# Performance work log

Hardware: AMD Instinct MI355X
Metric: run time of the kernel (lower is better)

## Reference

```python
import jax, jax.numpy as jnp
import numpy as np
import math

D_MODEL = 512
NUM_HEADS = 8
D_K = D_MODEL // NUM_HEADS
B, S = 8, 2048


def setup_inputs() -> dict:
    key = jax.random.key(0)
    ks = jax.random.split(key, 13)
    inv = 1.0 / math.sqrt(D_MODEL)
    def lin(kw, kb):
        W = jax.random.uniform(kw, (D_MODEL, D_MODEL), jnp.float32, -inv, inv)
        b = jax.random.uniform(kb, (D_MODEL,), jnp.float32, -inv, inv)
        return W, b
    Wq, bq = lin(ks[0], ks[1])
    Wk, bk = lin(ks[2], ks[3])
    Wv, bv = lin(ks[4], ks[5])
    Wo, bo = lin(ks[6], ks[7])
    Q = jax.random.normal(ks[8], (B, S, D_MODEL), jnp.float32)
    K = jax.random.normal(ks[9], (B, S, D_MODEL), jnp.float32)
    V = jax.random.normal(ks[10], (B, S, D_MODEL), jnp.float32)
    mask = jax.random.randint(ks[11], (1, 1, S, S), 0, 2, jnp.int32)
    return {"Q": Q, "K": K, "V": V, "mask": mask,
            "Wq": Wq, "bq": bq, "Wk": Wk, "bk": bk,
            "Wv": Wv, "bv": bv, "Wo": Wo, "bo": bo}


def _split_heads(x):
    b, s, _ = x.shape
    return x.reshape(b, s, NUM_HEADS, D_K).transpose(0, 2, 1, 3)  # [B,H,S,dk]


def reference(Q, K, V, mask, Wq, bq, Wk, bk, Wv, bv, Wo, bo):
    # Linear projections (torch Linear: x @ W^T + b) then head split
    q = _split_heads(Q @ Wq.T + bq)
    k = _split_heads(K @ Wk.T + bk)
    v = _split_heads(V @ Wv.T + bv)
    scores = jnp.einsum("bhqd,bhkd->bhqk", q, k) / math.sqrt(D_K)
    # masked_fill(mask == 0, -1e30) for float32
    scores = jnp.where(mask == 0, jnp.float32(-1e30), scores)
    probs = jax.nn.softmax(scores, axis=-1)
    # dropout in eval mode == identity
    out = jnp.einsum("bhqk,bhkd->bhqd", probs, v)
    out = out.transpose(0, 2, 1, 3).reshape(Q.shape[0], -1, D_MODEL)
    return out @ Wo.T + bo
```

## Files before the change

kernel.cpp:

```cpp
#include <hip/hip_runtime.h>
#include <hip/hip_bf16.h>
#include <math.h>

#define BB 8
#define SS 2048
#define HH 8
#define DKK 64
#define DM 512

typedef short bf16x8 __attribute__((ext_vector_type(8)));
typedef short bf16x4 __attribute__((ext_vector_type(4)));
typedef float f32x4 __attribute__((ext_vector_type(4)));
#define MFMA16(a, b, c) __builtin_amdgcn_mfma_f32_16x16x32_bf16(a, b, c, 0, 0, 0)

#if __has_builtin(__builtin_amdgcn_exp2f)
#define EXP2(x) __builtin_amdgcn_exp2f(x)
#else
#define EXP2(x) exp2f(x)
#endif

__device__ __forceinline__ unsigned short f2bf(float f) {
    __hip_bfloat16 h = __float2bfloat16(f);
    return *reinterpret_cast<unsigned short*>(&h);
}

__device__ __forceinline__ uint4 cvt8(const float* __restrict__ src) {
    float4 a = *(const float4*)src;
    float4 b = *(const float4*)(src + 4);
    unsigned short tmp[8];
    tmp[0] = f2bf(a.x); tmp[1] = f2bf(a.y); tmp[2] = f2bf(a.z); tmp[3] = f2bf(a.w);
    tmp[4] = f2bf(b.x); tmp[5] = f2bf(b.y); tmp[6] = f2bf(b.z); tmp[7] = f2bf(b.w);
    return *(uint4*)tmp;
}

__global__ __launch_bounds__(256) void mask_pack(
    const int* __restrict__ mask, unsigned long long* __restrict__ mb)
{
    const int t = threadIdx.x;
    const int wid = (blockIdx.x << 2) | (t >> 6);
    const int lane = t & 63;
    const int q = wid >> 5;
    const int c = wid & 31;
    int e = mask[(size_t)q * SS + (c << 6) + lane];
    unsigned long long bal = __ballot(e != 0);
    if (lane == 0) mb[wid] = bal;
}

__global__ __launch_bounds__(256, 2) void proj_qkv_fused(
    const float* __restrict__ Xq, const float* __restrict__ Xk, const float* __restrict__ Xv,
    const float* __restrict__ Wq, const float* __restrict__ Wk, const float* __restrict__ Wv,
    const float* __restrict__ bq, const float* __restrict__ bk, const float* __restrict__ bv,
    unsigned short* __restrict__ outbase, float qscale)
{
    const int z = blockIdx.z;
    const float* X = (z == 0) ? Xq : (z == 1) ? Xk : Xv;
    const float* W = (z == 0) ? Wq : (z == 1) ? Wk : Wv;
    const float* bias = (z == 0) ? bq : (z == 1) ? bk : bv;
    unsigned short* out = outbase + (size_t)z * ((size_t)BB * HH * SS * DKK);
    const float scale = (z == 0) ? qscale : 1.0f;

    __shared__ __align__(16) unsigned short Xs[128][72];
    __shared__ __align__(16) unsigned short Ws[128][72];
    const int t = threadIdx.x;
    const int w = t >> 6, l = t & 63;
    const int l15 = l & 15, lg = l >> 4;
    const int n0 = blockIdx.x * 128, m0 = blockIdx.y * 128;
    const int mo = (w & 1) * 64, no = (w >> 1) * 64;

    f32x4 acc[4][4];
#pragma unroll
    for (int i = 0; i < 4; i++)
#pragma unroll
        for (int j = 0; j < 4; j++) acc[i][j] = (f32x4){0.f, 0.f, 0.f, 0.f};

    for (int k0 = 0; k0 < DM; k0 += 64) {
        __syncthreads();
#pragma unroll
        for (int rr = 0; rr < 4; rr++) {
            int idx = rr * 2048 + t * 8;
            int row = idx >> 6, col = idx & 63;
            *(uint4*)&Xs[row][col] = cvt8(X + (size_t)(m0 + row) * DM + k0 + col);
            *(uint4*)&Ws[row][col] = cvt8(W + (size_t)(n0 + row) * DM + k0 + col);
        }
        __syncthreads();

        bf16x8 af[4][2], bfr[4][2];
#pragma unroll
        for (int mt = 0; mt < 4; mt++) {
            af[mt][0] = *(const bf16x8*)&Xs[mo + mt * 16 + l15][lg * 8];
            af[mt][1] = *(const bf16x8*)&Xs[mo + mt * 16 + l15][32 + lg * 8];
        }
#pragma unroll
        for (int nt = 0; nt < 4; nt++) {
            bfr[nt][0] = *(const bf16x8*)&Ws[no + nt * 16 + l15][lg * 8];
            bfr[nt][1] = *(const bf16x8*)&Ws[no + nt * 16 + l15][32 + lg * 8];
        }
#pragma unroll
        for (int mt = 0; mt < 4; mt++)
#pragma unroll
            for (int nt = 0; nt < 4; nt++) {
                acc[mt][nt] = MFMA16(af[mt][0], bfr[nt][0], acc[mt][nt]);
                acc[mt][nt] = MFMA16(af[mt][1], bfr[nt][1], acc[mt][nt]);
            }
    }

    float bv4[4];
#pragma unroll
    for (int nt = 0; nt < 4; nt++) bv4[nt] = bias[n0 + no + nt * 16 + l15];

    const int h = (n0 + no) >> 6;
    if (z == 2) {
#pragma unroll
        for (int mt = 0; mt < 4; mt++) {
            int m = m0 + mo + mt * 16 + lg * 4;
            int bb = m >> 11, s = m & (SS - 1);
#pragma unroll
            for (int nt = 0; nt < 4; nt++) {
                int d = nt * 16 + l15;
                bf16x4 pk;
#pragma unroll
                for (int r = 0; r < 4; r++) pk[r] = (short)f2bf(acc[mt][nt][r] + bv4[nt]);
                *(bf16x4*)(out + (((size_t)bb * HH + h) * DKK + d) * SS + s) = pk;
            }
        }
    } else {
#pragma unroll
        for (int mt = 0; mt < 4; mt++)
#pragma unroll
            for (int nt = 0; nt < 4; nt++)
#pragma unroll
                for (int r = 0; r < 4; r++) {
                    int m = m0 + mo + mt * 16 + lg * 4 + r;
                    int d = nt * 16 + l15;
                    float v = (acc[mt][nt][r] + bv4[nt]) * scale;
                    int bb = m >> 11, s = m & (SS - 1);
                    out[(((size_t)bb * HH + h) * SS + s) * 64 + d] = f2bf(v);
                }
    }
}

__global__ __launch_bounds__(256, 2) void proj_out_mfma(
    const unsigned short* __restrict__ Xb,
    const float* __restrict__ W,
    const float* __restrict__ bias,
    float* __restrict__ out)
{
    __shared__ __align__(16) unsigned short Xs[128][72];
    __shared__ __align__(16) unsigned short Ws[128][72];
    const int t = threadIdx.x;
    const int w = t >> 6, l = t & 63;
    const int l15 = l & 15, lg = l >> 4;
    const int n0 = blockIdx.x * 128, m0 = blockIdx.y * 128;
    const int mo = (w & 1) * 64, no = (w >> 1) * 64;

    f32x4 acc[4][4];
#pragma unroll
    for (int i = 0; i < 4; i++)
#pragma unroll
        for (int j = 0; j < 4; j++) acc[i][j] = (f32x4){0.f, 0.f, 0.f, 0.f};

    for (int k0 = 0; k0 < DM; k0 += 64) {
        __syncthreads();
#pragma unroll
        for (int rr = 0; rr < 4; rr++) {
            int idx = rr * 2048 + t * 8;
            int row = idx >> 6, col = idx & 63;
            *(uint4*)&Xs[row][col] = *(const uint4*)(Xb + (size_t)(m0 + row) * DM + k0 + col);
            *(uint4*)&Ws[row][col] = cvt8(W + (size_t)(n0 + row) * DM + k0 + col);
        }
        __syncthreads();

        bf16x8 af[4][2], bfr[4][2];
#pragma unroll
        for (int mt = 0; mt < 4; mt++) {
            af[mt][0] = *(const bf16x8*)&Xs[mo + mt * 16 + l15][lg * 8];
            af[mt][1] = *(const bf16x8*)&Xs[mo + mt * 16 + l15][32 + lg * 8];
        }
#pragma unroll
        for (int nt = 0; nt < 4; nt++) {
            bfr[nt][0] = *(const bf16x8*)&Ws[no + nt * 16 + l15][lg * 8];
            bfr[nt][1] = *(const bf16x8*)&Ws[no + nt * 16 + l15][32 + lg * 8];
        }
#pragma unroll
        for (int mt = 0; mt < 4; mt++)
#pragma unroll
            for (int nt = 0; nt < 4; nt++) {
                acc[mt][nt] = MFMA16(af[mt][0], bfr[nt][0], acc[mt][nt]);
                acc[mt][nt] = MFMA16(af[mt][1], bfr[nt][1], acc[mt][nt]);
            }
    }

    float bv4[4];
#pragma unroll
    for (int nt = 0; nt < 4; nt++) bv4[nt] = bias[n0 + no + nt * 16 + l15];

#pragma unroll
    for (int mt = 0; mt < 4; mt++)
#pragma unroll
        for (int nt = 0; nt < 4; nt++)
#pragma unroll
            for (int r = 0; r < 4; r++) {
                int m = m0 + mo + mt * 16 + lg * 4 + r;
                int n = n0 + no + nt * 16 + l15;
                out[(size_t)m * DM + n] = acc[mt][nt][r] + bv4[nt];
            }
}

__global__ __launch_bounds__(256, 2) void attn_kernel(
    const unsigned short* __restrict__ qw, const unsigned short* __restrict__ kw,
    const unsigned short* __restrict__ vtw,
    const unsigned long long* __restrict__ mb,
    unsigned short* __restrict__ ao)
{
    __shared__ __align__(16) unsigned short Ks[64][72];
    __shared__ __align__(16) unsigned short Vt[64][72];
    __shared__ __align__(16) unsigned short Pw[4 * 64 * 64];
    const int t = threadIdx.x;
    const int w = t >> 6, l = t & 63;
    const int l15 = l & 15, lg = l >> 4;
    const int q0 = blockIdx.x * 256;
    const int bh = blockIdx.y;
    const int b = bh >> 3, h = bh & 7;
    const int q0w = q0 + w * 64;
    const unsigned short* qb = qw + (size_t)bh * SS * DKK;
    const unsigned short* kb = kw + (size_t)bh * SS * DKK;
    const unsigned short* vtb = vtw + (size_t)bh * DKK * SS;

    const unsigned long long* mbq[4];
#pragma unroll
    for (int qt = 0; qt < 4; qt++)
        mbq[qt] = mb + ((size_t)(q0w + qt * 16 + l15) << 5);

    bf16x8 Qf[4][2];
#pragma unroll
    for (int qt = 0; qt < 4; qt++)
#pragma unroll
        for (int dh = 0; dh < 2; dh++)
            Qf[qt][dh] = *(const bf16x8*)(qb + (size_t)(q0w + qt * 16 + l15) * DKK + dh * 32 + lg * 8);

    f32x4 O[4][4];
#pragma unroll
    for (int i = 0; i < 4; i++)
#pragma unroll
        for (int j = 0; j < 4; j++) O[i][j] = (f32x4){0.f, 0.f, 0.f, 0.f};
    float m_i[4], l_i[4];
#pragma unroll
    for (int i = 0; i < 4; i++) { m_i[i] = -INFINITY; l_i[i] = 0.f; }

    const int pbase = w * 4096;

    for (int kv0 = 0; kv0 < SS; kv0 += 64) {
        __syncthreads();
#pragma unroll
        for (int r = 0; r < 2; r++) {
            int idx = r * 2048 + t * 8;
            int row = idx >> 6, col = idx & 63;
            *(uint4*)&Ks[row][col] = *(const uint4*)(kb + (size_t)(kv0 + row) * DKK + col);
            *(uint4*)&Vt[row][col] = *(const uint4*)(vtb + (size_t)row * SS + kv0 + col);
        }
        __syncthreads();

        f32x4 S[4][4];
#pragma unroll
        for (int kvt = 0; kvt < 4; kvt++) {
            bf16x8 ak0 = *(const bf16x8*)&Ks[kvt * 16 + l15][lg * 8];
            bf16x8 ak1 = *(const bf16x8*)&Ks[kvt * 16 + l15][32 + lg * 8];
#pragma unroll
            for (int qt = 0; qt < 4; qt++) {
                f32x4 z = (f32x4){0.f, 0.f, 0.f, 0.f};
                z = MFMA16(ak0, Qf[qt][0], z);
                z = MFMA16(ak1, Qf[qt][1], z);
                S[kvt][qt] = z;
            }
        }

#pragma unroll
        for (int qt = 0; qt < 4; qt++) {
            unsigned long long mm = mbq[qt][kv0 >> 6];
            unsigned int wlo = (unsigned int)mm;
            unsigned int whi = (unsigned int)(mm >> 32);
            unsigned int u[4];
            u[0] = wlo >> (lg * 4);
            u[1] = wlo >> (16 + lg * 4);
            u[2] = whi >> (lg * 4);
            u[3] = whi >> (16 + lg * 4);
#pragma unroll
            for (int kvt = 0; kvt < 4; kvt++) {
                if (!(u[kvt] & 1u)) S[kvt][qt][0] = -1e38f;
                if (!(u[kvt] & 2u)) S[kvt][qt][1] = -1e38f;
                if (!(u[kvt] & 4u)) S[kvt][qt][2] = -1e38f;
                if (!(u[kvt] & 8u)) S[kvt][qt][3] = -1e38f;
            }
        }

        float mtl[4];
#pragma unroll
        for (int qt = 0; qt < 4; qt++) {
            float mt = S[0][qt][0];
#pragma unroll
            for (int kvt = 0; kvt < 4; kvt++)
#pragma unroll
                for (int r = 0; r < 4; r++) mt = fmaxf(mt, S[kvt][qt][r]);
            mt = fmaxf(mt, __shfl_xor(mt, 16));
            mt = fmaxf(mt, __shfl_xor(mt, 32));
            mtl[qt] = mt;
        }
        int grow = (mtl[0] > m_i[0]) | (mtl[1] > m_i[1]) |
                   (mtl[2] > m_i[2]) | (mtl[3] > m_i[3]);
        if (__any(grow)) {
            float alpha[4];
#pragma unroll
            for (int qt = 0; qt < 4; qt++) {
                float mn = fmaxf(m_i[qt], mtl[qt]);
                alpha[qt] = EXP2(m_i[qt] - mn);
                m_i[qt] = mn;
                l_i[qt] *= alpha[qt];
            }
#pragma unroll
            for (int qt = 0; qt < 4; qt++)
#pragma unroll
                for (int r = 0; r < 4; r++) {
                    float a = __shfl(alpha[qt], lg * 4 + r);
#pragma unroll
                    for (int dt = 0; dt < 4; dt++) O[qt][dt][r] *= a;
                }
        }

#pragma unroll
        for (int qt = 0; qt < 4; qt++) {
            float ls = 0.f;
            const int prow = qt * 16 + l15;
            const int swz = (prow & 7) << 3;
#pragma unroll
            for (int kvt = 0; kvt < 4; kvt++) {
                float p0 = EXP2(S[kvt][qt][0] - m_i[qt]);
                float p1 = EXP2(S[kvt][qt][1] - m_i[qt]);
                float p2 = EXP2(S[kvt][qt][2] - m_i[qt]);
                float p3 = EXP2(S[kvt][qt][3] - m_i[qt]);
                ls += (p0 + p1) + (p2 + p3);
                bf16x4 pk;
                pk[0] = (short)f2bf(p0); pk[1] = (short)f2bf(p1);
                pk[2] = (short)f2bf(p2); pk[3] = (short)f2bf(p3);
                *(bf16x4*)&Pw[pbase + prow * 64 + ((kvt * 16 + lg * 4) ^ swz)] = pk;
            }
            ls += __shfl_xor(ls, 16);
            ls += __shfl_xor(ls, 32);
            l_i[qt] += ls;
        }

        asm volatile("s_waitcnt lgkmcnt(0)" ::: "memory");

        bf16x8 bv2[4][2];
#pragma unroll
        for (int dt = 0; dt < 4; dt++) {
            bv2[dt][0] = *(const bf16x8*)&Vt[dt * 16 + l15][lg * 8];
            bv2[dt][1] = *(const bf16x8*)&Vt[dt * 16 + l15][32 + lg * 8];
        }
#pragma unroll
        for (int qt = 0; qt < 4; qt++) {
            const int prow = qt * 16 + l15;
            const int swz = (prow & 7) << 3;
            bf16x8 ap0 = *(const bf16x8*)&Pw[pbase + prow * 64 + ((lg * 8) ^ swz)];
            bf16x8 ap1 = *(const bf16x8*)&Pw[pbase + prow * 64 + ((32 + lg * 8) ^ swz)];
#pragma unroll
            for (int dt = 0; dt < 4; dt++) {
                O[qt][dt] = MFMA16(ap0, bv2[dt][0], O[qt][dt]);
                O[qt][dt] = MFMA16(ap1, bv2[dt][1], O[qt][dt]);
            }
        }
    }

#pragma unroll
    for (int qt = 0; qt < 4; qt++) {
        float li = 1.f / l_i[qt];
#pragma unroll
        for (int r = 0; r < 4; r++) {
            float lv = __shfl(li, lg * 4 + r);
            int q = q0w + qt * 16 + lg * 4 + r;
            size_t base = ((size_t)b * SS + q) * DM + h * 64;
#pragma unroll
            for (int dt = 0; dt < 4; dt++)
                ao[base + dt * 16 + l15] = f2bf(O[qt][dt][r] * lv);
        }
    }
}

extern "C" void kernel_launch(void* const* d_in, const int* in_sizes, int n_in,
                              void* d_out, int out_size, void* d_ws, size_t ws_size,
                              hipStream_t stream) {
    const float* Q    = (const float*)d_in[0];
    const float* K    = (const float*)d_in[1];
    const float* V    = (const float*)d_in[2];
    const int*   mask = (const int*)d_in[3];
    const float* Wq   = (const float*)d_in[4];
    const float* bq   = (const float*)d_in[5];
    const float* Wk   = (const float*)d_in[6];
    const float* bk   = (const float*)d_in[7];
    const float* Wv   = (const float*)d_in[8];
    const float* bv   = (const float*)d_in[9];
    const float* Wo   = (const float*)d_in[10];
    const float* bo   = (const float*)d_in[11];

    const size_t SEG = (size_t)BB * HH * SS * DKK;
    unsigned short* qb  = (unsigned short*)d_ws;
    unsigned short* kb  = qb + SEG;
    unsigned short* vtb = kb + SEG;
    unsigned short* ab  = vtb + SEG;

    const size_t MB_BYTES = (size_t)SS * (SS / 64) * sizeof(unsigned long long);
    unsigned long long* mbits =
        (unsigned long long*)((char*)d_out + (size_t)out_size - MB_BYTES);

    const float qscale = 0.125f * 1.44269504088896340736f;

    mask_pack<<<dim3((SS * (SS / 64)) / 4), 256, 0, stream>>>(mask, mbits);

    dim3 gp(DM / 128, (BB * SS) / 128, 3);
    proj_qkv_fused<<<gp, 256, 0, stream>>>(Q, K, V, Wq, Wk, Wv, bq, bk, bv, qb, qscale);

    attn_kernel<<<dim3(SS / 256, BB * HH), 256, 0, stream>>>(qb, kb, vtb, mbits, ab);

    proj_out_mfma<<<dim3(DM / 128, (BB * SS) / 128), 256, 0, stream>>>(ab, Wo, bo, (float*)d_out);
}
```

Before: 407.8 us.

## Halve attention query tile, compute row sums via MFMA, pre-convert QKV weights

The attention kernel now handles 32 queries per wave instead of 64 and launches twice as many blocks. This cuts register and shared-memory use per block so more blocks can run per CU, at the cost of reloading K and V twice as often. The softmax denominator now comes from an extra MFMA of P against a vector of ones, replacing the scalar sum and shuffles, and the row max uses a max3 tree. A new kernel converts Wq, Wk and Wv to bf16 once, into workspace that is later overwritten by the attention output, so the projection kernel loads bf16 weights directly instead of converting them inside every tile.

Result: faster. 392.6 us (-3.7%).

```diff
diff --git a/kernel.cpp b/kernel.cpp
--- a/kernel.cpp
+++ b/kernel.cpp
@@ -22,6 +22,10 @@
 __device__ __forceinline__ unsigned short f2bf(float f) {
     __hip_bfloat16 h = __float2bfloat16(f);
     return *reinterpret_cast<unsigned short*>(&h);
+}
+
+__device__ __forceinline__ float max3f(float a, float b, float c) {
+    return fmaxf(fmaxf(a, b), c);
 }
 
 __device__ __forceinline__ uint4 cvt8(const float* __restrict__ src) {
@@ -46,15 +50,26 @@
     if (lane == 0) mb[wid] = bal;
 }
 
+__global__ __launch_bounds__(256) void w_cvt(
+    const float* __restrict__ Wq, const float* __restrict__ Wk,
+    const float* __restrict__ Wv, unsigned short* __restrict__ dst)
+{
+    const int idx = blockIdx.x * 256 + threadIdx.x;
+    const int which = idx >> 15;
+    const int off = (idx & 32767) * 8;
+    const float* src = (which == 0) ? Wq : (which == 1) ? Wk : Wv;
+    *(uint4*)(dst + (size_t)which * 262144 + off) = cvt8(src + off);
+}
+
 __global__ __launch_bounds__(256, 2) void proj_qkv_fused(
     const float* __restrict__ Xq, const float* __restrict__ Xk, const float* __restrict__ Xv,
-    const float* __restrict__ Wq, const float* __restrict__ Wk, const float* __restrict__ Wv,
+    const unsigned short* __restrict__ Wb,
     const float* __restrict__ bq, const float* __restrict__ bk, const float* __restrict__ bv,
     unsigned short* __restrict__ outbase, float qscale)
 {
     const int z = blockIdx.z;
     const float* X = (z == 0) ? Xq : (z == 1) ? Xk : Xv;
-    const float* W = (z == 0) ? Wq : (z == 1) ? Wk : Wv;
+    const unsigned short* W = Wb + (size_t)z * 262144;
     const float* bias = (z == 0) ? bq : (z == 1) ? bk : bv;
     unsigned short* out = outbase + (size_t)z * ((size_t)BB * HH * SS * DKK);
     const float scale = (z == 0) ? qscale : 1.0f;
@@ -80,7 +95,7 @@
             int idx = rr * 2048 + t * 8;
             int row = idx >> 6, col = idx & 63;
             *(uint4*)&Xs[row][col] = cvt8(X + (size_t)(m0 + row) * DM + k0 + col);
-            *(uint4*)&Ws[row][col] = cvt8(W + (size_t)(n0 + row) * DM + k0 + col);
+            *(uint4*)&Ws[row][col] = *(const uint4*)(W + (size_t)(n0 + row) * DM + k0 + col);
         }
         __syncthreads();
 
@@ -214,40 +229,44 @@
 {
     __shared__ __align__(16) unsigned short Ks[64][72];
     __shared__ __align__(16) unsigned short Vt[64][72];
-    __shared__ __align__(16) unsigned short Pw[4 * 64 * 64];
+    __shared__ __align__(16) unsigned short Pw[4 * 32 * 64];
     const int t = threadIdx.x;
     const int w = t >> 6, l = t & 63;
     const int l15 = l & 15, lg = l >> 4;
-    const int q0 = blockIdx.x * 256;
+    const int q0 = blockIdx.x * 128;
     const int bh = blockIdx.y;
     const int b = bh >> 3, h = bh & 7;
-    const int q0w = q0 + w * 64;
+    const int q0w = q0 + w * 32;
     const unsigned short* qb = qw + (size_t)bh * SS * DKK;
     const unsigned short* kb = kw + (size_t)bh * SS * DKK;
     const unsigned short* vtb = vtw + (size_t)bh * DKK * SS;
 
-    const unsigned long long* mbq[4];
-#pragma unroll
-    for (int qt = 0; qt < 4; qt++)
+    const unsigned long long* mbq[2];
+#pragma unroll
+    for (int qt = 0; qt < 2; qt++)
         mbq[qt] = mb + ((size_t)(q0w + qt * 16 + l15) << 5);
 
-    bf16x8 Qf[4][2];
-#pragma unroll
-    for (int qt = 0; qt < 4; qt++)
+    bf16x8 Qf[2][2];
+#pragma unroll
+    for (int qt = 0; qt < 2; qt++)
 #pragma unroll
         for (int dh = 0; dh < 2; dh++)
             Qf[qt][dh] = *(const bf16x8*)(qb + (size_t)(q0w + qt * 16 + l15) * DKK + dh * 32 + lg * 8);
 
-    f32x4 O[4][4];
-#pragma unroll
-    for (int i = 0; i < 4; i++)
+    f32x4 O[2][4];
+    f32x4 Osum[2];
+#pragma unroll
+    for (int i = 0; i < 2; i++) {
 #pragma unroll
         for (int j = 0; j < 4; j++) O[i][j] = (f32x4){0.f, 0.f, 0.f, 0.f};
-    float m_i[4], l_i[4];
-#pragma unroll
-    for (int i = 0; i < 4; i++) { m_i[i] = -INFINITY; l_i[i] = 0.f; }
-
-    const int pbase = w * 4096;
+        Osum[i] = (f32x4){0.f, 0.f, 0.f, 0.f};
+    }
+    float m_i[2];
+#pragma unroll
+    for (int i = 0; i < 2; i++) m_i[i] = -INFINITY;
+
+    const bf16x8 vone = {16256, 16256, 16256, 16256, 16256, 16256, 16256, 16256};
+    const int pbase = w * 2048;
 
     for (int kv0 = 0; kv0 < SS; kv0 += 64) {
         __syncthreads();
@@ -260,13 +279,13 @@
         }
         __syncthreads();
 
-        f32x4 S[4][4];
+        f32x4 S[4][2];
 #pragma unroll
         for (int kvt = 0; kvt < 4; kvt++) {
             bf16x8 ak0 = *(const bf16x8*)&Ks[kvt * 16 + l15][lg * 8];
             bf16x8 ak1 = *(const bf16x8*)&Ks[kvt * 16 + l15][32 + lg * 8];
 #pragma unroll
-            for (int qt = 0; qt < 4; qt++) {
+            for (int qt = 0; qt < 2; qt++) {
                 f32x4 z = (f32x4){0.f, 0.f, 0.f, 0.f};
                 z = MFMA16(ak0, Qf[qt][0], z);
                 z = MFMA16(ak1, Qf[qt][1], z);
@@ -275,7 +294,7 @@
         }
 
 #pragma unroll
-        for (int qt = 0; qt < 4; qt++) {
+        for (int qt = 0; qt < 2; qt++) {
             unsigned long long mm = mbq[qt][kv0 >> 6];
             unsigned int wlo = (unsigned int)mm;
             unsigned int whi = (unsigned int)(mm >> 32);
@@ -293,42 +312,41 @@
             }
         }
 
-        float mtl[4];
-#pragma unroll
-        for (int qt = 0; qt < 4; qt++) {
-            float mt = S[0][qt][0];
-#pragma unroll
-            for (int kvt = 0; kvt < 4; kvt++)
-#pragma unroll
-                for (int r = 0; r < 4; r++) mt = fmaxf(mt, S[kvt][qt][r]);
+        float mtl[2];
+#pragma unroll
+        for (int qt = 0; qt < 2; qt++) {
+            float mt = fmaxf(
+                max3f(max3f(S[0][qt][0], S[0][qt][1], S[0][qt][2]),
+                      max3f(S[0][qt][3], S[1][qt][0], S[1][qt][1]),
+                      max3f(S[1][qt][2], S[1][qt][3], S[2][qt][0])),
+                fmaxf(max3f(S[2][qt][1], S[2][qt][2], S[2][qt][3]),
+                      max3f(S[3][qt][0], S[3][qt][1], fmaxf(S[3][qt][2], S[3][qt][3]))));
             mt = fmaxf(mt, __shfl_xor(mt, 16));
             mt = fmaxf(mt, __shfl_xor(mt, 32));
             mtl[qt] = mt;
         }
-        int grow = (mtl[0] > m_i[0]) | (mtl[1] > m_i[1]) |
-                   (mtl[2] > m_i[2]) | (mtl[3] > m_i[3]);
+        int grow = (mtl[0] > m_i[0]) | (mtl[1] > m_i[1]);
         if (__any(grow)) {
-            float alpha[4];
-#pragma unroll
-            for (int qt = 0; qt < 4; qt++) {
+            float alpha[2];
+#pragma unroll
+            for (int qt = 0; qt < 2; qt++) {
                 float mn = fmaxf(m_i[qt], mtl[qt]);
                 alpha[qt] = EXP2(m_i[qt] - mn);
                 m_i[qt] = mn;
-                l_i[qt] *= alpha[qt];
-            }
-#pragma unroll
-            for (int qt = 0; qt < 4; qt++)
+            }
+#pragma unroll
+            for (int qt = 0; qt < 2; qt++)
 #pragma unroll
                 for (int r = 0; r < 4; r++) {
                     float a = __shfl(alpha[qt], lg * 4 + r);
 #pragma unroll
                     for (int dt = 0; dt < 4; dt++) O[qt][dt][r] *= a;
+                    Osum[qt][r] *= a;
                 }
         }
 
 #pragma unroll
-        for (int qt = 0; qt < 4; qt++) {
-            float ls = 0.f;
+        for (int qt = 0; qt < 2; qt++) {
             const int prow = qt * 16 + l15;
             const int swz = (prow & 7) << 3;
 #pragma unroll
@@ -337,15 +355,11 @@
                 float p1 = EXP2(S[kvt][qt][1] - m_i[qt]);
                 float p2 = EXP2(S[kvt][qt][2] - m_i[qt]);
                 float p3 = EXP2(S[kvt][qt][3] - m_i[qt]);
-                ls += (p0 + p1) + (p2 + p3);
                 bf16x4 pk;
                 pk[0] = (short)f2bf(p0); pk[1] = (short)f2bf(p1);
                 pk[2] = (short)f2bf(p2); pk[3] = (short)f2bf(p3);
                 *(bf16x4*)&Pw[pbase + prow * 64 + ((kvt * 16 + lg * 4) ^ swz)] = pk;
             }
-            ls += __shfl_xor(ls, 16);
-            ls += __shfl_xor(ls, 32);
-            l_i[qt] += ls;
         }
 
         asm volatile("s_waitcnt lgkmcnt(0)" ::: "memory");
@@ -357,7 +371,7 @@
             bv2[dt][1] = *(const bf16x8*)&Vt[dt * 16 + l15][32 + lg * 8];
         }
 #pragma unroll
-        for (int qt = 0; qt < 4; qt++) {
+        for (int qt = 0; qt < 2; qt++) {
             const int prow = qt * 16 + l15;
             const int swz = (prow & 7) << 3;
             bf16x8 ap0 = *(const bf16x8*)&Pw[pbase + prow * 64 + ((lg * 8) ^ swz)];
@@ -367,15 +381,16 @@
                 O[qt][dt] = MFMA16(ap0, bv2[dt][0], O[qt][dt]);
                 O[qt][dt] = MFMA16(ap1, bv2[dt][1], O[qt][dt]);
             }
-        }
-    }
-
-#pragma unroll
-    for (int qt = 0; qt < 4; qt++) {
-        float li = 1.f / l_i[qt];
+            Osum[qt] = MFMA16(ap0, vone, Osum[qt]);
+            Osum[qt] = MFMA16(ap1, vone, Osum[qt]);
+        }
+    }
+
+#pragma unroll
+    for (int qt = 0; qt < 2; qt++) {
 #pragma unroll
         for (int r = 0; r < 4; r++) {
-            float lv = __shfl(li, lg * 4 + r);
+            float lv = 1.f / Osum[qt][r];
             int q = q0w + qt * 16 + lg * 4 + r;
             size_t base = ((size_t)b * SS + q) * DM + h * 64;
 #pragma unroll
@@ -406,6 +421,7 @@
     unsigned short* kb  = qb + SEG;
     unsigned short* vtb = kb + SEG;
     unsigned short* ab  = vtb + SEG;
+    unsigned short* wb  = ab;
 
     const size_t MB_BYTES = (size_t)SS * (SS / 64) * sizeof(unsigned long long);
     unsigned long long* mbits =
@@ -414,11 +430,12 @@
     const float qscale = 0.125f * 1.44269504088896340736f;
 
     mask_pack<<<dim3((SS * (SS / 64)) / 4), 256, 0, stream>>>(mask, mbits);
+    w_cvt<<<dim3(384), 256, 0, stream>>>(Wq, Wk, Wv, wb);
 
     dim3 gp(DM / 128, (BB * SS) / 128, 3);
-    proj_qkv_fused<<<gp, 256, 0, stream>>>(Q, K, V, Wq, Wk, Wv, bq, bk, bv, qb, qscale);
-
-    attn_kernel<<<dim3(SS / 256, BB * HH), 256, 0, stream>>>(qb, kb, vtb, mbits, ab);
+    proj_qkv_fused<<<gp, 256, 0, stream>>>(Q, K, V, wb, bq, bk, bv, qb, qscale);
+
+    attn_kernel<<<dim3(SS / 128, BB * HH), 256, 0, stream>>>(qb, kb, vtb, mbits, ab);
 
     proj_out_mfma<<<dim3(DM / 128, (BB * SS) / 128), 256, 0, stream>>>(ab, Wo, bo, (float*)d_out);
 }
```
